# Performance work log

Hardware: AMD Instinct MI355X
Metric: run time of the kernel (lower is better)

## Reference

```python
import jax, jax.numpy as jnp
import numpy as np

N_SAMPLES = 5        # samples_per_num
N_ITERS = 10         # n_iter_sinkhorn
TEMP = 1.0
NOISE_FACTOR = 1.0
EPS = 1e-20

def setup_inputs() -> dict:
    key = jax.random.key(0)
    ks = jax.random.split(key, 6)
    B, n, latent = 512, 128, 128
    x = jax.random.normal(ks[0], (B, n), dtype=jnp.float32)
    w1 = jax.random.normal(ks[1], (latent, 1), dtype=jnp.float32) * (1.0)
    b1 = jax.random.normal(ks[2], (latent,), dtype=jnp.float32) * 0.1
    w2 = jax.random.normal(ks[3], (n, latent), dtype=jnp.float32) * (1.0 / np.sqrt(latent))
    b2 = jax.random.normal(ks[4], (n,), dtype=jnp.float32) * 0.1
    # Gumbel(0,1) noise for samples_per_num * B matrices
    u = jax.random.uniform(ks[5], (N_SAMPLES * B, n, n), dtype=jnp.float32)
    noise = -jnp.log(-jnp.log(u + EPS) + EPS)
    return {"x": x, "w1": w1, "b1": b1, "w2": w2, "b2": b2, "noise": noise}

def reference(x, w1, b1, w2, b2, noise):
    B, n = x.shape
    # per-scalar MLP: [B*n, 1] -> [B*n, latent] -> [B*n, n]
    h = jax.nn.relu(x.reshape(-1, 1) @ w1.T + b1)
    log_alpha = (h @ w2.T + b2).reshape(B, n, n)
    # tile across samples, add gumbel noise, divide by temperature
    la = jnp.tile(log_alpha, (N_SAMPLES, 1, 1))          # [S*B, n, n]
    la = (la + noise * NOISE_FACTOR) / TEMP
    # Sinkhorn: alternating row/column logsumexp normalization in log space
    def step(la, _):
        la = la - jax.scipy.special.logsumexp(la, axis=2, keepdims=True)
        la = la - jax.scipy.special.logsumexp(la, axis=1, keepdims=True)
        return la, None
    la, _ = jax.lax.scan(step, la, None, length=N_ITERS)
    # soft_perms_inf: exp, view [S,B,n,n], transpose(0,1) -> [B,S,n,n]
    # inv_soft_pers_flattened: transpose last two dims, transpose(0,1) back, flatten
    inv = jnp.exp(la).reshape(N_SAMPLES, B, n, n).transpose(0, 1, 3, 2)
    return inv.reshape(-1, n, n)                          # [S*B, n, n]
```

## Files before the change

### kernel.cpp

```cpp
#include <hip/hip_runtime.h>

#define NN   128
#define NB   512
#define NMAT 2560
#define L2E  1.4426950408889634f

typedef __attribute__((ext_vector_type(4))) float  f32x4;
typedef __attribute__((ext_vector_type(4))) int    i32x4;
typedef __attribute__((ext_vector_type(8))) ushort u16x8;

__device__ __forceinline__ float fexp2(float x){ float r; asm("v_exp_f32 %0, %1" : "=v"(r) : "v"(x)); return r; }
__device__ __forceinline__ float flog2(float x){ float r; asm("v_log_f32 %0, %1" : "=v"(r) : "v"(x)); return r; }
__device__ __forceinline__ float frcp (float x){ float r; asm("v_rcp_f32 %0, %1" : "=v"(r) : "v"(x)); return r; }

__device__ __forceinline__ ushort f2bf(float f){
    unsigned u = __float_as_uint(f);
    unsigned r = (u + 0x7FFFu + ((u >> 16) & 1u)) >> 16;
    return (ushort)r;
}
__device__ __forceinline__ float bf2f(ushort h){ return __uint_as_float(((unsigned)h) << 16); }

#define MFMA16(acc, a, b) \
    asm("v_mfma_f32_16x16x32_bf16 %0, %1, %2, %0" : "+v"(acc) : "v"(a), "v"(b))

__global__ __launch_bounds__(256) void prep_kernel(
    const float* __restrict__ w2, const float* __restrict__ b2,
    ushort* __restrict__ Bhi, ushort* __restrict__ Blo, float* __restrict__ b2s)
{
    int fid = blockIdx.x * 256 + threadIdx.x;
    int ct = fid >> 8, ks = (fid >> 6) & 3, lane = fid & 63;
    int c  = ct * 16 + (lane & 15);
    int k0 = ks * 32 + ((lane >> 4) << 3);
    u16x8 hi, lo;
#pragma unroll
    for (int j = 0; j < 8; j++) {
        float v = w2[c * NN + k0 + j] * L2E;
        ushort h = f2bf(v);
        hi[j] = h;
        lo[j] = f2bf(v - bf2f(h));
    }
    *(u16x8*)(Bhi + (size_t)fid * 8) = hi;
    *(u16x8*)(Blo + (size_t)fid * 8) = lo;
    if (fid < NN) b2s[fid] = b2[fid] * L2E;
}

__global__ __launch_bounds__(256) void mlp_mfma_kernel(
    const float* __restrict__ x,  const float* __restrict__ w1,
    const float* __restrict__ b1, const ushort* __restrict__ Bhi,
    const ushort* __restrict__ Blo, const float* __restrict__ b2s,
    float* __restrict__ la)
{
    const int t    = threadIdx.x;
    const int w    = t >> 6;
    const int lane = t & 63;
    const int blk  = blockIdx.x;
    const int b    = blk >> 1;
    const int rh   = blk & 1;

    const int r = rh * 64 + w * 16 + (lane & 15);
    const float xv = x[b * NN + r];

    i32x4 Ahi[4], Alo[4];
#pragma unroll
    for (int ks = 0; ks < 4; ks++) {
        const int l0 = ks * 32 + ((lane >> 4) << 3);
        float4 w1a = *(const float4*)(w1 + l0);
        float4 w1b = *(const float4*)(w1 + l0 + 4);
        float4 b1a = *(const float4*)(b1 + l0);
        float4 b1b = *(const float4*)(b1 + l0 + 4);
        float h[8];
        h[0] = fmaxf(fmaf(xv, w1a.x, b1a.x), 0.f);
        h[1] = fmaxf(fmaf(xv, w1a.y, b1a.y), 0.f);
        h[2] = fmaxf(fmaf(xv, w1a.z, b1a.z), 0.f);
        h[3] = fmaxf(fmaf(xv, w1a.w, b1a.w), 0.f);
        h[4] = fmaxf(fmaf(xv, w1b.x, b1b.x), 0.f);
        h[5] = fmaxf(fmaf(xv, w1b.y, b1b.y), 0.f);
        h[6] = fmaxf(fmaf(xv, w1b.z, b1b.z), 0.f);
        h[7] = fmaxf(fmaf(xv, w1b.w, b1b.w), 0.f);
#pragma unroll
        for (int p = 0; p < 4; p++) {
            ushort h0 = f2bf(h[2 * p]);
            ushort h1 = f2bf(h[2 * p + 1]);
            ushort l0e = f2bf(h[2 * p]     - bf2f(h0));
            ushort l1e = f2bf(h[2 * p + 1] - bf2f(h1));
            ((int*)&Ahi[ks])[p] = ((int)h1 << 16) | (int)h0;
            ((int*)&Alo[ks])[p] = ((int)l1e << 16) | (int)l0e;
        }
    }

    f32x4 acc[8];
#pragma unroll
    for (int ct = 0; ct < 8; ct++) acc[ct] = (f32x4){0.f, 0.f, 0.f, 0.f};

    asm volatile("s_nop 7");

#pragma unroll
    for (int ks = 0; ks < 4; ks++) {
#pragma unroll
        for (int ct = 0; ct < 8; ct++) {
            const size_t off = ((size_t)(ct * 4 + ks) * 64 + lane) * 8;
            i32x4 bh = *(const i32x4*)(Bhi + off);
            i32x4 bl = *(const i32x4*)(Blo + off);
            MFMA16(acc[ct], Ahi[ks], bh);
            MFMA16(acc[ct], Ahi[ks], bl);
            MFMA16(acc[ct], Alo[ks], bh);
        }
    }

    asm volatile("s_nop 7");
    asm volatile("s_nop 7");
    asm volatile("s_nop 3");

    const int row0 = b * NN + rh * 64 + w * 16 + (lane >> 4) * 4;
    const int col  = lane & 15;
#pragma unroll
    for (int ct = 0; ct < 8; ct++) {
        float bb = b2s[ct * 16 + col];
        float* lp = la + (size_t)row0 * NN + ct * 16 + col;
#pragma unroll
        for (int q = 0; q < 4; q++)
            lp[(size_t)q * NN] = acc[ct][q] + bb;
    }
}

__global__ __launch_bounds__(512, 6) void sinkhorn_kernel(
    const float* __restrict__ la, const float* __restrict__ noise,
    float* __restrict__ out)
{
    __shared__ float part[8][132];
    __shared__ float tbuf[128];

    const int m    = blockIdx.x;
    const int b    = m & (NB - 1);
    const int t    = threadIdx.x;
    const int wv   = t >> 6;
    const int lane = t & 63;
    const int tr   = t >> 4, tc = t & 15;
    const int r0   = tr * 4,  c0 = tc * 8;

    const float* lab = la    + (size_t)b * NN * NN;
    const float* nb  = noise + (size_t)m * NN * NN;

    float E[4][8];
#pragma unroll
    for (int i = 0; i < 4; i++) {
        const float* lr = lab + (r0 + i) * NN + c0;
        const float* nr = nb  + (r0 + i) * NN + c0;
        float4 a0 = *(const float4*)(lr);
        float4 a1 = *(const float4*)(lr + 4);
        float4 n0 = *(const float4*)(nr);
        float4 n1 = *(const float4*)(nr + 4);
        E[i][0] = fmaf(n0.x, L2E, a0.x);
        E[i][1] = fmaf(n0.y, L2E, a0.y);
        E[i][2] = fmaf(n0.z, L2E, a0.z);
        E[i][3] = fmaf(n0.w, L2E, a0.w);
        E[i][4] = fmaf(n1.x, L2E, a1.x);
        E[i][5] = fmaf(n1.y, L2E, a1.y);
        E[i][6] = fmaf(n1.z, L2E, a1.z);
        E[i][7] = fmaf(n1.w, L2E, a1.w);
    }

#pragma unroll
    for (int i = 0; i < 4; i++) {
        float mx = E[i][0];
#pragma unroll
        for (int j = 1; j < 8; j++) mx = fmaxf(mx, E[i][j]);
#pragma unroll
        for (int s = 1; s < 16; s <<= 1) mx = fmaxf(mx, __shfl_xor(mx, s));
        float sm = 0.f;
#pragma unroll
        for (int j = 0; j < 8; j++) sm += fexp2(E[i][j] - mx);
#pragma unroll
        for (int s = 1; s < 16; s <<= 1) sm += __shfl_xor(sm, s);
        float R1 = mx + flog2(sm);
#pragma unroll
        for (int j = 0; j < 8; j++) E[i][j] = fexp2(E[i][j] - R1);
    }

    float u[4];
#pragma unroll
    for (int i = 0; i < 4; i++) u[i] = 1.f;
    float tj[8];

    for (int k = 0; k < 10; k++) {
        float loc[8];
#pragma unroll
        for (int j = 0; j < 8; j++) {
            float s = 0.f;
#pragma unroll
            for (int i = 0; i < 4; i++) s = fmaf(E[i][j], u[i], s);
            loc[j] = s;
        }
#pragma unroll
        for (int j = 0; j < 8; j++) {
            loc[j] += __shfl_xor(loc[j], 16);
            loc[j] += __shfl_xor(loc[j], 32);
        }
        if (lane < 16) {
            *(float4*)&part[wv][c0]     = make_float4(loc[0], loc[1], loc[2], loc[3]);
            *(float4*)&part[wv][c0 + 4] = make_float4(loc[4], loc[5], loc[6], loc[7]);
        }
        __syncthreads();
        if (t < NN) {
            float cs = part[0][t];
#pragma unroll
            for (int p = 1; p < 8; p++) cs += part[p][t];
            tbuf[t] = frcp(cs);
        }
        __syncthreads();
        {
            float4 t0 = *(const float4*)&tbuf[c0];
            float4 t1 = *(const float4*)&tbuf[c0 + 4];
            tj[0] = t0.x; tj[1] = t0.y; tj[2] = t0.z; tj[3] = t0.w;
            tj[4] = t1.x; tj[5] = t1.y; tj[6] = t1.z; tj[7] = t1.w;
        }
        if (k < 9) {
#pragma unroll
            for (int i = 0; i < 4; i++) {
                float s = 0.f;
#pragma unroll
                for (int j = 0; j < 8; j++) s = fmaf(E[i][j], tj[j], s);
#pragma unroll
                for (int sf = 1; sf < 16; sf <<= 1) s += __shfl_xor(s, sf);
                u[i] = frcp(s);
            }
        }
    }

    float* ob = out + (size_t)m * NN * NN;
#pragma unroll
    for (int j = 0; j < 8; j++) {
        float4 v;
        v.x = E[0][j] * u[0] * tj[j];
        v.y = E[1][j] * u[1] * tj[j];
        v.z = E[2][j] * u[2] * tj[j];
        v.w = E[3][j] * u[3] * tj[j];
        *(float4*)(ob + (size_t)(c0 + j) * NN + r0) = v;
    }
}

extern "C" void kernel_launch(void* const* d_in, const int* in_sizes, int n_in,
                              void* d_out, int out_size, void* d_ws, size_t ws_size,
                              hipStream_t stream) {
    const float* x     = (const float*)d_in[0];
    const float* w1    = (const float*)d_in[1];
    const float* b1    = (const float*)d_in[2];
    const float* w2    = (const float*)d_in[3];
    const float* b2    = (const float*)d_in[4];
    const float* noise = (const float*)d_in[5];
    float* out = (float*)d_out;

    char* ws  = (char*)d_ws;
    float*  la  = (float*)ws;
    ushort* Bhi = (ushort*)(ws + 33554432);
    ushort* Blo = (ushort*)(ws + 33554432 + 32768);
    float*  b2s = (float*)(ws + 33554432 + 65536);

    hipLaunchKernelGGL(prep_kernel, dim3(8), dim3(256), 0, stream,
                       w2, b2, Bhi, Blo, b2s);
    hipLaunchKernelGGL(mlp_mfma_kernel, dim3(1024), dim3(256), 0, stream,
                       x, w1, b1, Bhi, Blo, b2s, la);
    hipLaunchKernelGGL(sinkhorn_kernel, dim3(NMAT), dim3(512), 0, stream,
                       la, noise, out);
}
```

Baseline: 138.2 us.

## Fuse MLP MFMA into Sinkhorn kernel, recomputing log_alpha per block

Merges the MLP kernel into the Sinkhorn kernel so each block computes its batch's log_alpha in registers via bf16 split MFMAs and adds noise directly. This removes the intermediate log_alpha workspace write and its re-read for every sample. The tile layout switches to the MFMA output layout, and the inline-asm intrinsics are replaced by compiler builtins. In exchange, the MLP is recomputed five times per batch, noise loads become scalar, and the launch bound allows fewer resident blocks.

```diff
diff --git a/kernel.cpp b/kernel.cpp
--- a/kernel.cpp
+++ b/kernel.cpp
@@ -6,12 +6,12 @@
 #define L2E  1.4426950408889634f
 
 typedef __attribute__((ext_vector_type(4))) float  f32x4;
-typedef __attribute__((ext_vector_type(4))) int    i32x4;
+typedef __attribute__((ext_vector_type(8))) short  short8;
 typedef __attribute__((ext_vector_type(8))) ushort u16x8;
 
-__device__ __forceinline__ float fexp2(float x){ float r; asm("v_exp_f32 %0, %1" : "=v"(r) : "v"(x)); return r; }
-__device__ __forceinline__ float flog2(float x){ float r; asm("v_log_f32 %0, %1" : "=v"(r) : "v"(x)); return r; }
-__device__ __forceinline__ float frcp (float x){ float r; asm("v_rcp_f32 %0, %1" : "=v"(r) : "v"(x)); return r; }
+__device__ __forceinline__ float fexp2(float x){ return __builtin_amdgcn_exp2f(x); }
+__device__ __forceinline__ float flog2(float x){ return __builtin_amdgcn_logf(x); }
+__device__ __forceinline__ float frcp (float x){ return __builtin_amdgcn_rcpf(x); }
 
 __device__ __forceinline__ ushort f2bf(float f){
     unsigned u = __float_as_uint(f);
@@ -20,8 +20,16 @@
 }
 __device__ __forceinline__ float bf2f(ushort h){ return __uint_as_float(((unsigned)h) << 16); }
 
-#define MFMA16(acc, a, b) \
-    asm("v_mfma_f32_16x16x32_bf16 %0, %1, %2, %0" : "+v"(acc) : "v"(a), "v"(b))
+__device__ __forceinline__ float red16(float x){
+#pragma unroll
+    for (int s = 1; s < 16; s <<= 1) x += __shfl_xor(x, s);
+    return x;
+}
+__device__ __forceinline__ float rmax16(float x){
+#pragma unroll
+    for (int s = 1; s < 16; s <<= 1) x = fmaxf(x, __shfl_xor(x, s));
+    return x;
+}
 
 __global__ __launch_bounds__(256) void prep_kernel(
     const float* __restrict__ w2, const float* __restrict__ b2,
@@ -44,198 +52,153 @@
     if (fid < NN) b2s[fid] = b2[fid] * L2E;
 }
 
-__global__ __launch_bounds__(256) void mlp_mfma_kernel(
-    const float* __restrict__ x,  const float* __restrict__ w1,
-    const float* __restrict__ b1, const ushort* __restrict__ Bhi,
+__global__ __launch_bounds__(512, 4) void fused_kernel(
+    const float* __restrict__ x,   const float* __restrict__ w1,
+    const float* __restrict__ b1,  const ushort* __restrict__ Bhi,
     const ushort* __restrict__ Blo, const float* __restrict__ b2s,
-    float* __restrict__ la)
+    const float* __restrict__ noise, float* __restrict__ out)
 {
+    __shared__ float part[8][132];
+    __shared__ float tbufT[128];
+
+    const int m    = blockIdx.x;
+    const int b    = m & (NB - 1);
     const int t    = threadIdx.x;
     const int w    = t >> 6;
     const int lane = t & 63;
-    const int blk  = blockIdx.x;
-    const int b    = blk >> 1;
-    const int rh   = blk & 1;
-
-    const int r = rh * 64 + w * 16 + (lane & 15);
-    const float xv = x[b * NN + r];
-
-    i32x4 Ahi[4], Alo[4];
+    const int h    = lane >> 4;
+    const int cc   = lane & 15;
+
+    const float* nb = noise + (size_t)m * NN * NN;
+    float* ob       = out   + (size_t)m * NN * NN;
+
+    const float xv = x[b * NN + 16 * w + cc];
+
+    short8 Ahi[4], Alo[4];
 #pragma unroll
     for (int ks = 0; ks < 4; ks++) {
-        const int l0 = ks * 32 + ((lane >> 4) << 3);
+        const int l0 = ks * 32 + (h << 3);
         float4 w1a = *(const float4*)(w1 + l0);
         float4 w1b = *(const float4*)(w1 + l0 + 4);
         float4 b1a = *(const float4*)(b1 + l0);
         float4 b1b = *(const float4*)(b1 + l0 + 4);
-        float h[8];
-        h[0] = fmaxf(fmaf(xv, w1a.x, b1a.x), 0.f);
-        h[1] = fmaxf(fmaf(xv, w1a.y, b1a.y), 0.f);
-        h[2] = fmaxf(fmaf(xv, w1a.z, b1a.z), 0.f);
-        h[3] = fmaxf(fmaf(xv, w1a.w, b1a.w), 0.f);
-        h[4] = fmaxf(fmaf(xv, w1b.x, b1b.x), 0.f);
-        h[5] = fmaxf(fmaf(xv, w1b.y, b1b.y), 0.f);
-        h[6] = fmaxf(fmaf(xv, w1b.z, b1b.z), 0.f);
-        h[7] = fmaxf(fmaf(xv, w1b.w, b1b.w), 0.f);
-#pragma unroll
-        for (int p = 0; p < 4; p++) {
-            ushort h0 = f2bf(h[2 * p]);
-            ushort h1 = f2bf(h[2 * p + 1]);
-            ushort l0e = f2bf(h[2 * p]     - bf2f(h0));
-            ushort l1e = f2bf(h[2 * p + 1] - bf2f(h1));
-            ((int*)&Ahi[ks])[p] = ((int)h1 << 16) | (int)h0;
-            ((int*)&Alo[ks])[p] = ((int)l1e << 16) | (int)l0e;
+        float hv[8];
+        hv[0] = fmaxf(fmaf(xv, w1a.x, b1a.x), 0.f);
+        hv[1] = fmaxf(fmaf(xv, w1a.y, b1a.y), 0.f);
+        hv[2] = fmaxf(fmaf(xv, w1a.z, b1a.z), 0.f);
+        hv[3] = fmaxf(fmaf(xv, w1a.w, b1a.w), 0.f);
+        hv[4] = fmaxf(fmaf(xv, w1b.x, b1b.x), 0.f);
+        hv[5] = fmaxf(fmaf(xv, w1b.y, b1b.y), 0.f);
+        hv[6] = fmaxf(fmaf(xv, w1b.z, b1b.z), 0.f);
+        hv[7] = fmaxf(fmaf(xv, w1b.w, b1b.w), 0.f);
+#pragma unroll
+        for (int j = 0; j < 8; j++) {
+            ushort hb = f2bf(hv[j]);
+            Ahi[ks][j] = (short)hb;
+            Alo[ks][j] = (short)f2bf(hv[j] - bf2f(hb));
         }
     }
 
     f32x4 acc[8];
 #pragma unroll
     for (int ct = 0; ct < 8; ct++) acc[ct] = (f32x4){0.f, 0.f, 0.f, 0.f};
-
-    asm volatile("s_nop 7");
 
 #pragma unroll
     for (int ks = 0; ks < 4; ks++) {
 #pragma unroll
         for (int ct = 0; ct < 8; ct++) {
             const size_t off = ((size_t)(ct * 4 + ks) * 64 + lane) * 8;
-            i32x4 bh = *(const i32x4*)(Bhi + off);
-            i32x4 bl = *(const i32x4*)(Blo + off);
-            MFMA16(acc[ct], Ahi[ks], bh);
-            MFMA16(acc[ct], Ahi[ks], bl);
-            MFMA16(acc[ct], Alo[ks], bh);
-        }
-    }
-
-    asm volatile("s_nop 7");
-    asm volatile("s_nop 7");
-    asm volatile("s_nop 3");
-
-    const int row0 = b * NN + rh * 64 + w * 16 + (lane >> 4) * 4;
-    const int col  = lane & 15;
+            short8 bh = *(const short8*)(Bhi + off);
+            short8 bl = *(const short8*)(Blo + off);
+            acc[ct] = __builtin_amdgcn_mfma_f32_16x16x32_bf16(Ahi[ks], bh, acc[ct], 0, 0, 0);
+            acc[ct] = __builtin_amdgcn_mfma_f32_16x16x32_bf16(Ahi[ks], bl, acc[ct], 0, 0, 0);
+            acc[ct] = __builtin_amdgcn_mfma_f32_16x16x32_bf16(Alo[ks], bh, acc[ct], 0, 0, 0);
+        }
+    }
+
+    float E[8][4];
+#pragma unroll
+    for (int ct = 0; ct < 8; ct++)
+#pragma unroll
+        for (int q = 0; q < 4; q++)
+            E[ct][q] = nb[(size_t)(16 * w + 4 * h + q) * NN + 16 * ct + cc];
+
 #pragma unroll
     for (int ct = 0; ct < 8; ct++) {
-        float bb = b2s[ct * 16 + col];
-        float* lp = la + (size_t)row0 * NN + ct * 16 + col;
+        float bb = b2s[16 * ct + cc];
 #pragma unroll
         for (int q = 0; q < 4; q++)
-            lp[(size_t)q * NN] = acc[ct][q] + bb;
-    }
-}
-
-__global__ __launch_bounds__(512, 6) void sinkhorn_kernel(
-    const float* __restrict__ la, const float* __restrict__ noise,
-    float* __restrict__ out)
-{
-    __shared__ float part[8][132];
-    __shared__ float tbuf[128];
-
-    const int m    = blockIdx.x;
-    const int b    = m & (NB - 1);
-    const int t    = threadIdx.x;
-    const int wv   = t >> 6;
-    const int lane = t & 63;
-    const int tr   = t >> 4, tc = t & 15;
-    const int r0   = tr * 4,  c0 = tc * 8;
-
-    const float* lab = la    + (size_t)b * NN * NN;
-    const float* nb  = noise + (size_t)m * NN * NN;
-
-    float E[4][8];
-#pragma unroll
-    for (int i = 0; i < 4; i++) {
-        const float* lr = lab + (r0 + i) * NN + c0;
-        const float* nr = nb  + (r0 + i) * NN + c0;
-        float4 a0 = *(const float4*)(lr);
-        float4 a1 = *(const float4*)(lr + 4);
-        float4 n0 = *(const float4*)(nr);
-        float4 n1 = *(const float4*)(nr + 4);
-        E[i][0] = fmaf(n0.x, L2E, a0.x);
-        E[i][1] = fmaf(n0.y, L2E, a0.y);
-        E[i][2] = fmaf(n0.z, L2E, a0.z);
-        E[i][3] = fmaf(n0.w, L2E, a0.w);
-        E[i][4] = fmaf(n1.x, L2E, a1.x);
-        E[i][5] = fmaf(n1.y, L2E, a1.y);
-        E[i][6] = fmaf(n1.z, L2E, a1.z);
-        E[i][7] = fmaf(n1.w, L2E, a1.w);
-    }
-
-#pragma unroll
-    for (int i = 0; i < 4; i++) {
-        float mx = E[i][0];
-#pragma unroll
-        for (int j = 1; j < 8; j++) mx = fmaxf(mx, E[i][j]);
-#pragma unroll
-        for (int s = 1; s < 16; s <<= 1) mx = fmaxf(mx, __shfl_xor(mx, s));
+            E[ct][q] = fmaf(E[ct][q], L2E, acc[ct][q] + bb);
+    }
+
+#pragma unroll
+    for (int q = 0; q < 4; q++) {
+        float mx = E[0][q];
+#pragma unroll
+        for (int ct = 1; ct < 8; ct++) mx = fmaxf(mx, E[ct][q]);
+        mx = rmax16(mx);
         float sm = 0.f;
 #pragma unroll
-        for (int j = 0; j < 8; j++) sm += fexp2(E[i][j] - mx);
-#pragma unroll
-        for (int s = 1; s < 16; s <<= 1) sm += __shfl_xor(sm, s);
+        for (int ct = 0; ct < 8; ct++) sm += fexp2(E[ct][q] - mx);
+        sm = red16(sm);
         float R1 = mx + flog2(sm);
 #pragma unroll
-        for (int j = 0; j < 8; j++) E[i][j] = fexp2(E[i][j] - R1);
+        for (int ct = 0; ct < 8; ct++) E[ct][q] = fexp2(E[ct][q] - R1);
     }
 
     float u[4];
 #pragma unroll
-    for (int i = 0; i < 4; i++) u[i] = 1.f;
+    for (int q = 0; q < 4; q++) u[q] = 1.f;
     float tj[8];
 
     for (int k = 0; k < 10; k++) {
         float loc[8];
 #pragma unroll
-        for (int j = 0; j < 8; j++) {
+        for (int ct = 0; ct < 8; ct++) {
             float s = 0.f;
 #pragma unroll
-            for (int i = 0; i < 4; i++) s = fmaf(E[i][j], u[i], s);
-            loc[j] = s;
-        }
-#pragma unroll
-        for (int j = 0; j < 8; j++) {
-            loc[j] += __shfl_xor(loc[j], 16);
-            loc[j] += __shfl_xor(loc[j], 32);
+            for (int q = 0; q < 4; q++) s = fmaf(E[ct][q], u[q], s);
+            s += __shfl_xor(s, 16);
+            s += __shfl_xor(s, 32);
+            loc[ct] = s;
         }
         if (lane < 16) {
-            *(float4*)&part[wv][c0]     = make_float4(loc[0], loc[1], loc[2], loc[3]);
-            *(float4*)&part[wv][c0 + 4] = make_float4(loc[4], loc[5], loc[6], loc[7]);
+            *(float4*)&part[w][cc * 8]     = make_float4(loc[0], loc[1], loc[2], loc[3]);
+            *(float4*)&part[w][cc * 8 + 4] = make_float4(loc[4], loc[5], loc[6], loc[7]);
         }
         __syncthreads();
         if (t < NN) {
             float cs = part[0][t];
 #pragma unroll
             for (int p = 1; p < 8; p++) cs += part[p][t];
-            tbuf[t] = frcp(cs);
+            tbufT[t] = frcp(cs);
         }
         __syncthreads();
         {
-            float4 t0 = *(const float4*)&tbuf[c0];
-            float4 t1 = *(const float4*)&tbuf[c0 + 4];
+            float4 t0 = *(const float4*)&tbufT[cc * 8];
+            float4 t1 = *(const float4*)&tbufT[cc * 8 + 4];
             tj[0] = t0.x; tj[1] = t0.y; tj[2] = t0.z; tj[3] = t0.w;
             tj[4] = t1.x; tj[5] = t1.y; tj[6] = t1.z; tj[7] = t1.w;
         }
         if (k < 9) {
 #pragma unroll
-            for (int i = 0; i < 4; i++) {
+            for (int q = 0; q < 4; q++) {
                 float s = 0.f;
 #pragma unroll
-                for (int j = 0; j < 8; j++) s = fmaf(E[i][j], tj[j], s);
-#pragma unroll
-                for (int sf = 1; sf < 16; sf <<= 1) s += __shfl_xor(s, sf);
-                u[i] = frcp(s);
+                for (int ct = 0; ct < 8; ct++) s = fmaf(E[ct][q], tj[ct], s);
+                u[q] = frcp(red16(s));
             }
         }
     }
 
-    float* ob = out + (size_t)m * NN * NN;
-#pragma unroll
-    for (int j = 0; j < 8; j++) {
+#pragma unroll
+    for (int ct = 0; ct < 8; ct++) {
         float4 v;
-        v.x = E[0][j] * u[0] * tj[j];
-        v.y = E[1][j] * u[1] * tj[j];
-        v.z = E[2][j] * u[2] * tj[j];
-        v.w = E[3][j] * u[3] * tj[j];
-        *(float4*)(ob + (size_t)(c0 + j) * NN + r0) = v;
+        v.x = E[ct][0] * u[0] * tj[ct];
+        v.y = E[ct][1] * u[1] * tj[ct];
+        v.z = E[ct][2] * u[2] * tj[ct];
+        v.w = E[ct][3] * u[3] * tj[ct];
+        *(float4*)(ob + (size_t)(16 * ct + cc) * NN + 16 * w + 4 * h) = v;
     }
 }
 
@@ -251,15 +214,12 @@
     float* out = (float*)d_out;
 
     char* ws  = (char*)d_ws;
-    float*  la  = (float*)ws;
-    ushort* Bhi = (ushort*)(ws + 33554432);
-    ushort* Blo = (ushort*)(ws + 33554432 + 32768);
-    float*  b2s = (float*)(ws + 33554432 + 65536);
+    ushort* Bhi = (ushort*)ws;
+    ushort* Blo = (ushort*)(ws + 32768);
+    float*  b2s = (float*)(ws + 65536);
 
     hipLaunchKernelGGL(prep_kernel, dim3(8), dim3(256), 0, stream,
                        w2, b2, Bhi, Blo, b2s);
-    hipLaunchKernelGGL(mlp_mfma_kernel, dim3(1024), dim3(256), 0, stream,
-                       x, w1, b1, Bhi, Blo, b2s, la);
-    hipLaunchKernelGGL(sinkhorn_kernel, dim3(NMAT), dim3(512), 0, stream,
-                       la, noise, out);
-}
+    hipLaunchKernelGGL(fused_kernel, dim3(NMAT), dim3(512), 0, stream,
+                       x, w1, b1, Bhi, Blo, b2s, noise, out);
+}
```

Measured after the change: 154.2 us. +11.6%, slower.
